# Optimization experiments

Measured on AMD Instinct MI355X. Metric: run time of the kernel, lower is better.

The kernel has to match this reference:

```python
import jax, jax.numpy as jnp
import numpy as np

H = 16  # n_heads


def setup_inputs() -> dict:
    key = jax.random.key(0)
    ks = jax.random.split(key, 11)
    B, S, D = 2, 2048, 1024
    def rn(k, shape, scale=1.0):
        return jax.random.normal(k, shape, dtype=jnp.float32) * scale
    w_scale = 1.0 / np.sqrt(D)
    return {
        "queries": rn(ks[0], (B, S, D)),
        "keys": rn(ks[1], (B, S, D)),
        "values": rn(ks[2], (B, S, D)),
        "Wq": rn(ks[3], (D, D), w_scale), "bq": rn(ks[4], (D,), 0.02),
        "Wk": rn(ks[5], (D, D), w_scale), "bk": rn(ks[6], (D,), 0.02),
        "Wv": rn(ks[7], (D, D), w_scale), "bv": rn(ks[8], (D,), 0.02),
        "Wo": rn(ks[9], (D, D), w_scale), "bo": rn(ks[10], (D,), 0.02),
    }


def _split_heads(x, h):
    # [B, S, D] -> [B, h, S, D/h]
    B, S, D = x.shape
    return x.reshape(B, S, h, D // h).transpose(0, 2, 1, 3)


def reference(queries, keys, values, Wq, bq, Wk, bk, Wv, bv, Wo, bo):
    B, S, D = queries.shape
    Q = _split_heads(queries @ Wq + bq, H)  # [B,h,S,dk]
    K = _split_heads(keys @ Wk + bk, H)
    V = _split_heads(values @ Wv + bv, H)
    # Faithful quirk: scale by sqrt(seq_len), not sqrt(d_k)
    factor = jnp.sqrt(jnp.asarray(S, dtype=Q.dtype))
    scores = jnp.einsum("bhqd,bhkd->bhqk", Q, K) / factor  # [B,h,S,S]
    weights = jax.nn.softmax(scores, axis=-1)
    attn = jnp.einsum("bhqk,bhkd->bhqd", weights, V)  # [B,h,S,dk]
    attn = attn.transpose(0, 2, 1, 3).reshape(B, S, D)  # [B,S,D]
    return attn @ Wo + bo
```

## Files before the change

### kernel.cpp

```cpp
#include <hip/hip_runtime.h>

typedef unsigned short ushort_t;
typedef unsigned int uint_t;
typedef __attribute__((ext_vector_type(8))) short short8;
typedef __attribute__((ext_vector_type(4))) float floatx4;

#define QSCALE 0.03187936f

__device__ __forceinline__ ushort_t f2bf(float f) {
    union { float f; uint_t u; } c; c.f = f;
    uint_t u = c.u;
    return (ushort_t)((u + 0x7fffu + ((u >> 16) & 1u)) >> 16);
}
__device__ __forceinline__ floatx4 mfma16x32(short8 a, short8 b, floatx4 c) {
    return __builtin_amdgcn_mfma_f32_16x16x32_bf16(a, b, c, 0, 0, 0);
}
__device__ __forceinline__ floatx4 zero4() { floatx4 z = {0.f, 0.f, 0.f, 0.f}; return z; }

__device__ __forceinline__ void gload16(const ushort_t* g, ushort_t* l) {
    __builtin_amdgcn_global_load_lds(
        (const __attribute__((address_space(1))) void*)g,
        (__attribute__((address_space(3))) void*)l, 16, 0, 0);
}

__global__ __launch_bounds__(256) void cvt_bf16(
    const float* __restrict__ s0, const float* __restrict__ s1,
    const float* __restrict__ s2, ushort_t* __restrict__ d0,
    ushort_t* __restrict__ d1, ushort_t* __restrict__ d2)
{
    const int which = blockIdx.x >> 11;
    const int blk = blockIdx.x & 2047;
    const float* src = (which == 0) ? s0 : (which == 1) ? s1 : s2;
    ushort_t* dst = (which == 0) ? d0 : (which == 1) ? d1 : d2;
    const int i = (blk * 256 + threadIdx.x) * 8;
    float4 f0 = *(const float4*)(src + i);
    float4 f1 = *(const float4*)(src + i + 4);
    __align__(16) ushort_t t[8];
    t[0] = f2bf(f0.x); t[1] = f2bf(f0.y); t[2] = f2bf(f0.z); t[3] = f2bf(f0.w);
    t[4] = f2bf(f1.x); t[5] = f2bf(f1.y); t[6] = f2bf(f1.z); t[7] = f2bf(f1.w);
    *(uint4*)(dst + i) = *(uint4*)t;
}

__global__ __launch_bounds__(256) void transpose_w(
    const float* __restrict__ W0, const float* __restrict__ W1,
    const float* __restrict__ W2, const float* __restrict__ W3,
    ushort_t* __restrict__ WT)
{
    __shared__ ushort_t tile[64][65];
    const float* W = (blockIdx.y == 0) ? W0 : (blockIdx.y == 1) ? W1
                   : (blockIdx.y == 2) ? W2 : W3;
    ushort_t* dst = WT + (size_t)blockIdx.y * (1024 * 1024);
    const int t = threadIdx.x;
    const int r = t >> 2, p = t & 3;
    const int j0 = (blockIdx.x & 15) << 6, k0 = (blockIdx.x >> 4) << 6;

    const float* src = W + (size_t)(k0 + r) * 1024 + j0 + p * 16;
    float4 f0 = *(const float4*)(src);
    float4 f1 = *(const float4*)(src + 4);
    float4 f2 = *(const float4*)(src + 8);
    float4 f3 = *(const float4*)(src + 12);
    ushort_t* tr = &tile[r][p * 16];
    tr[0] = f2bf(f0.x); tr[1] = f2bf(f0.y); tr[2]  = f2bf(f0.z); tr[3]  = f2bf(f0.w);
    tr[4] = f2bf(f1.x); tr[5] = f2bf(f1.y); tr[6]  = f2bf(f1.z); tr[7]  = f2bf(f1.w);
    tr[8] = f2bf(f2.x); tr[9] = f2bf(f2.y); tr[10] = f2bf(f2.z); tr[11] = f2bf(f2.w);
    tr[12] = f2bf(f3.x); tr[13] = f2bf(f3.y); tr[14] = f2bf(f3.z); tr[15] = f2bf(f3.w);
    __syncthreads();
    __align__(16) ushort_t buf[16];
#pragma unroll
    for (int i = 0; i < 16; ++i) buf[i] = tile[p * 16 + i][r];
    ushort_t* o = dst + (size_t)(j0 + r) * 1024 + k0 + p * 16;
    *(uint4*)(o)     = *(uint4*)(buf);
    *(uint4*)(o + 8) = *(uint4*)(buf + 8);
}

__global__ __launch_bounds__(256) void gemm_bt(
    const ushort_t* __restrict__ A0, const ushort_t* __restrict__ A1,
    const ushort_t* __restrict__ A2, const ushort_t* __restrict__ WT,
    const float* __restrict__ b0, const float* __restrict__ b1,
    const float* __restrict__ b2,
    ushort_t* __restrict__ Dq, ushort_t* __restrict__ Dk,
    ushort_t* __restrict__ Dv, int zbase)
{
    __shared__ __align__(16) ushort_t As[128 * 32];
    __shared__ __align__(16) ushort_t Bs[128 * 32];

    const int mode = blockIdx.z + zbase;
    const ushort_t* A = (mode == 0) ? A0 : (mode == 1) ? A1 : A2;
    const float* bias = (mode == 0) ? b0 : (mode == 1) ? b1 : b2;
    const ushort_t* Bt = WT + (size_t)mode * 1048576;

    const int tid = threadIdx.x;
    const int lane = tid & 63, wid = tid >> 6;
    const int quad = lane >> 4, l16 = lane & 15;
    const int wm = wid >> 1, wn = wid & 1;
    const int row0 = blockIdx.y << 7, col0 = blockIdx.x << 7;

    floatx4 acc[4][4];
#pragma unroll
    for (int i = 0; i < 4; ++i)
#pragma unroll
        for (int j = 0; j < 4; ++j) acc[i][j] = zero4();

    const int i0 = tid, i1 = 256 + tid;
    const int r0_ = i0 >> 2, c0_ = (i0 & 3) ^ (r0_ & 3);
    const int r1_ = i1 >> 2, c1_ = (i1 & 3) ^ (r1_ & 3);
    const ushort_t* gA0 = A  + (size_t)(row0 + r0_) * 1024 + c0_ * 8;
    const ushort_t* gA1 = A  + (size_t)(row0 + r1_) * 1024 + c1_ * 8;
    const ushort_t* gB0 = Bt + (size_t)(col0 + r0_) * 1024 + c0_ * 8;
    const ushort_t* gB1 = Bt + (size_t)(col0 + r1_) * 1024 + c1_ * 8;
    ushort_t* lA0 = As + i0 * 8;  ushort_t* lA1 = As + i1 * 8;
    ushort_t* lB0 = Bs + i0 * 8;  ushort_t* lB1 = Bs + i1 * 8;

    const int ra = wm * 64 + l16, rb = wn * 64 + l16;
    const int sa_off = (quad ^ (l16 & 3)) * 8;

    for (int k0 = 0; k0 < 1024; k0 += 32) {
        __syncthreads();
        gload16(gA0 + k0, lA0);
        gload16(gA1 + k0, lA1);
        gload16(gB0 + k0, lB0);
        gload16(gB1 + k0, lB1);
        __syncthreads();

        short8 af[4], bf[4];
#pragma unroll
        for (int i = 0; i < 4; ++i)
            af[i] = *(const short8*)(As + (ra + i * 16) * 32 + sa_off);
#pragma unroll
        for (int j = 0; j < 4; ++j)
            bf[j] = *(const short8*)(Bs + (rb + j * 16) * 32 + sa_off);
#pragma unroll
        for (int i = 0; i < 4; ++i)
#pragma unroll
            for (int j = 0; j < 4; ++j)
                acc[i][j] = mfma16x32(af[i], bf[j], acc[i][j]);
    }

    const float sc = (mode == 0) ? QSCALE : 1.f;
#pragma unroll
    for (int i = 0; i < 4; ++i) {
#pragma unroll
        for (int j = 0; j < 4; ++j) {
            const int c = col0 + wn * 64 + j * 16 + l16;
            const float bv = bias[c];
#pragma unroll
            for (int rr = 0; rr < 4; ++rr) {
                const int r = row0 + wm * 64 + i * 16 + quad * 4 + rr;
                const float v = (acc[i][j][rr] + bv) * sc;
                const int b = r >> 11, s = r & 2047, h = c >> 6, d = c & 63;
                if (mode <= 1) {
                    ushort_t* D = (mode == 0) ? Dq : Dk;
                    D[(((b * 16 + h) * 2048 + s) << 6) + d] = f2bf(v);
                } else {
                    Dv[(((b * 16 + h) * 64 + d) << 11) + s] = f2bf(v);
                }
            }
        }
    }
}

__global__ __launch_bounds__(256) void gemm64(
    const ushort_t* __restrict__ A, const ushort_t* __restrict__ Bt,
    const float* __restrict__ bias, float* __restrict__ Dout)
{
    __shared__ __align__(16) ushort_t As[64 * 32];
    __shared__ __align__(16) ushort_t Bs[128 * 32];
    const int tid = threadIdx.x;
    const int lane = tid & 63, wid = tid >> 6;
    const int quad = lane >> 4, l16 = lane & 15;
    const int wm = wid >> 1, wn = wid & 1;
    const int row0 = blockIdx.y << 6, col0 = blockIdx.x << 7;

    floatx4 acc[2][4];
#pragma unroll
    for (int i = 0; i < 2; ++i)
#pragma unroll
        for (int j = 0; j < 4; ++j) acc[i][j] = zero4();

    const int rA = tid >> 2, cA = (tid & 3) ^ (rA & 3);
    const ushort_t* gA = A + (size_t)(row0 + rA) * 1024 + cA * 8;
    ushort_t* lA = As + tid * 8;
    const int i0 = tid, i1 = 256 + tid;
    const int rB0 = i0 >> 2, cB0 = (i0 & 3) ^ (rB0 & 3);
    const int rB1 = i1 >> 2, cB1 = (i1 & 3) ^ (rB1 & 3);
    const ushort_t* gB0 = Bt + (size_t)(col0 + rB0) * 1024 + cB0 * 8;
    const ushort_t* gB1 = Bt + (size_t)(col0 + rB1) * 1024 + cB1 * 8;
    ushort_t* lB0 = Bs + i0 * 8;  ushort_t* lB1 = Bs + i1 * 8;

    const int sa_off = (quad ^ (l16 & 3)) * 8;

    for (int k0 = 0; k0 < 1024; k0 += 32) {
        __syncthreads();
        gload16(gA + k0, lA);
        gload16(gB0 + k0, lB0);
        gload16(gB1 + k0, lB1);
        __syncthreads();

        short8 af[2], bf[4];
#pragma unroll
        for (int i = 0; i < 2; ++i)
            af[i] = *(const short8*)(As + (wm * 32 + i * 16 + l16) * 32 + sa_off);
#pragma unroll
        for (int j = 0; j < 4; ++j)
            bf[j] = *(const short8*)(Bs + (wn * 64 + j * 16 + l16) * 32 + sa_off);
#pragma unroll
        for (int i = 0; i < 2; ++i)
#pragma unroll
            for (int j = 0; j < 4; ++j)
                acc[i][j] = mfma16x32(af[i], bf[j], acc[i][j]);
    }

#pragma unroll
    for (int i = 0; i < 2; ++i)
#pragma unroll
        for (int j = 0; j < 4; ++j) {
            const int c = col0 + wn * 64 + j * 16 + l16;
            const float bv = bias[c];
#pragma unroll
            for (int rr = 0; rr < 4; ++rr) {
                const int r = row0 + wm * 32 + i * 16 + quad * 4 + rr;
                Dout[(size_t)r * 1024 + c] = acc[i][j][rr] + bv;
            }
        }
}

__global__ __launch_bounds__(256, 4) void attn64(
    const ushort_t* __restrict__ Q, const ushort_t* __restrict__ K,
    const ushort_t* __restrict__ Vt, ushort_t* __restrict__ Out)
{
    __shared__ __align__(16) ushort_t Ks[64 * 64];
    __shared__ __align__(16) ushort_t Vs[64 * 64];

    const int tid = threadIdx.x;
    const int lane = tid & 63, wid = tid >> 6;
    const int quad = lane >> 4, l16 = lane & 15;
    const int bh = blockIdx.y;
    const int q0 = blockIdx.x << 6;

    const ushort_t* Qh = Q + (size_t)bh * (2048 * 64);
    const ushort_t* Kh = K + (size_t)bh * (2048 * 64);
    const ushort_t* Vh = Vt + (size_t)bh * (64 * 2048);

    const int qr = q0 + wid * 16 + l16;
    const short8 qf0 = *(const short8*)(Qh + (size_t)qr * 64 + quad * 8);
    const short8 qf1 = *(const short8*)(Qh + (size_t)qr * 64 + 32 + quad * 8);

    float l_st = 0.f;
    floatx4 o_acc[4];
#pragma unroll
    for (int d = 0; d < 4; ++d) o_acc[d] = zero4();

    const int i0 = tid, i1 = 256 + tid;
    const int kr0 = i0 >> 3, kc0 = (i0 & 7) ^ (kr0 & 7);
    const int kr1 = i1 >> 3, kc1 = (i1 & 7) ^ (kr1 & 7);
    const ushort_t* gK0 = Kh + (size_t)kr0 * 64 + kc0 * 8;
    const ushort_t* gK1 = Kh + (size_t)kr1 * 64 + kc1 * 8;
    const ushort_t* gV0 = Vh + (size_t)kr0 * 2048 + kc0 * 8;
    const ushort_t* gV1 = Vh + (size_t)kr1 * 2048 + kc1 * 8;
    ushort_t* lK0 = Ks + i0 * 8;  ushort_t* lK1 = Ks + i1 * 8;
    ushort_t* lV0 = Vs + i0 * 8;  ushort_t* lV1 = Vs + i1 * 8;

    const int l7 = l16 & 7;
    const int q2 = quad >> 1, q1 = (quad & 1) * 4;

    for (int kt = 0; kt < 2048; kt += 64) {
        __syncthreads();
        gload16(gK0 + (size_t)kt * 64, lK0);
        gload16(gK1 + (size_t)kt * 64, lK1);
        gload16(gV0 + kt, lV0);
        gload16(gV1 + kt, lV1);
        __syncthreads();

        floatx4 sa[4];
#pragma unroll
        for (int g = 0; g < 4; ++g) {
            const int row = g * 16 + l16;
            const short8 kf0 = *(const short8*)(Ks + row * 64 + ((quad ^ l7) * 8));
            const short8 kf1 = *(const short8*)(Ks + row * 64 + (((quad + 4) ^ l7) * 8));
            sa[g] = mfma16x32(kf0, qf0, zero4());
            sa[g] = mfma16x32(kf1, qf1, sa[g]);
        }

#pragma unroll
        for (int G = 0; G < 2; ++G) {
            uint_t ub[8];
#pragma unroll
            for (int t = 0; t < 8; ++t) {
                const int g = G * 2 + (t >> 2), r = t & 3;
                const float e = __builtin_amdgcn_exp2f(fminf(sa[g][r], 80.f));
                const uint_t u = __float_as_uint(e) & 0xffff0000u;
                l_st += __uint_as_float(u);
                ub[t] = u;
            }
            union { uint_t u[4]; short8 s; } pc;
            pc.u[0] = (ub[0] >> 16) | ub[1];
            pc.u[1] = (ub[2] >> 16) | ub[3];
            pc.u[2] = (ub[4] >> 16) | ub[5];
            pc.u[3] = (ub[6] >> 16) | ub[7];
            const short8 pf = pc.s;

            const int ch0 = ((4 * G + q2) ^ l7) * 8;
            const int ch1 = ((4 * G + 2 + q2) ^ l7) * 8;
#pragma unroll
            for (int db = 0; db < 4; ++db) {
                const int vbase = (db * 16 + l16) * 64 + q1;
                const uint2 v0 = *(const uint2*)(Vs + vbase + ch0);
                const uint2 v1 = *(const uint2*)(Vs + vbase + ch1);
                union { uint_t u[4]; short8 s; } vc;
                vc.u[0] = v0.x; vc.u[1] = v0.y; vc.u[2] = v1.x; vc.u[3] = v1.y;
                o_acc[db] = mfma16x32(pf, vc.s, o_acc[db]);
            }
        }
    }

    l_st += __shfl_xor(l_st, 16);
    l_st += __shfl_xor(l_st, 32);

    const int b = bh >> 4, h = bh & 15;
    const int s0 = q0 + wid * 16 + quad * 4;
#pragma unroll
    for (int r = 0; r < 4; ++r) {
        const float lr = __shfl(l_st, quad * 4 + r);
        const float inv = 1.f / lr;
#pragma unroll
        for (int db = 0; db < 4; ++db) {
            const float v = o_acc[db][r] * inv;
            Out[(size_t)(b * 2048 + s0 + r) * 1024 + h * 64 + db * 16 + l16] = f2bf(v);
        }
    }
}

extern "C" void kernel_launch(void* const* d_in, const int* in_sizes, int n_in,
                              void* d_out, int out_size, void* d_ws, size_t ws_size,
                              hipStream_t stream) {
    const float* queries = (const float*)d_in[0];
    const float* keys    = (const float*)d_in[1];
    const float* values  = (const float*)d_in[2];
    const float* Wq = (const float*)d_in[3];
    const float* bq = (const float*)d_in[4];
    const float* Wk = (const float*)d_in[5];
    const float* bk = (const float*)d_in[6];
    const float* Wv = (const float*)d_in[7];
    const float* bv = (const float*)d_in[8];
    const float* Wo = (const float*)d_in[9];
    const float* bo = (const float*)d_in[10];
    float* out = (float*)d_out;

    char* ws = (char*)d_ws;
    const size_t MB = 1024 * 1024;
    ushort_t* WT = (ushort_t*)(ws);
    const ushort_t* WoT = WT + 3 * 1048576;
    dim3 tb(256);

    transpose_w<<<dim3(256, 4), tb, 0, stream>>>(Wq, Wk, Wv, Wo, WT);

    if (ws_size >= 64 * MB) {
        ushort_t* Qb  = (ushort_t*)(ws + 8 * MB);
        ushort_t* Kb  = (ushort_t*)(ws + 16 * MB);
        ushort_t* Vb  = (ushort_t*)(ws + 24 * MB);
        ushort_t* Qp  = (ushort_t*)(ws + 32 * MB);
        ushort_t* Kp  = (ushort_t*)(ws + 40 * MB);
        ushort_t* Vtp = (ushort_t*)(ws + 48 * MB);
        ushort_t* An  = (ushort_t*)(ws + 56 * MB);
        cvt_bf16<<<dim3(6144), tb, 0, stream>>>(queries, keys, values, Qb, Kb, Vb);
        gemm_bt<<<dim3(8, 32, 3), tb, 0, stream>>>(Qb, Kb, Vb, WT,
            bq, bk, bv, Qp, Kp, Vtp, 0);
        attn64<<<dim3(32, 32), tb, 0, stream>>>(Qp, Kp, Vtp, An);
        gemm64<<<dim3(8, 64), tb, 0, stream>>>(An, WoT, bo, out);
    } else {
        ushort_t* buf1 = (ushort_t*)(ws + 8 * MB);
        ushort_t* buf2 = (ushort_t*)(ws + 16 * MB);
        ushort_t* Qp   = (ushort_t*)(ws + 24 * MB);
        ushort_t* Kp   = (ushort_t*)(ws + 32 * MB);
        cvt_bf16<<<dim3(4096), tb, 0, stream>>>(queries, keys, keys, buf1, buf2, buf2);
        gemm_bt<<<dim3(8, 32, 2), tb, 0, stream>>>(buf1, buf2, buf2, WT,
            bq, bk, bk, Qp, Kp, Kp, 0);
        cvt_bf16<<<dim3(2048), tb, 0, stream>>>(values, values, values, buf1, buf1, buf1);
        gemm_bt<<<dim3(8, 32, 1), tb, 0, stream>>>(buf1, buf1, buf1, WT,
            bv, bv, bv, buf2, buf2, buf2, 2);
        attn64<<<dim3(32, 32), tb, 0, stream>>>(Qp, Kp, buf2, buf1);
        gemm64<<<dim3(8, 64), tb, 0, stream>>>(buf1, WoT, bo, out);
    }
}
```

Before: 237.3 us.

## Unify projection GEMMs on 64x128 tiles and widen attention KV tile to 128

Result: slower. 305.5 us (+28.7%).

```diff
diff --git a/kernel.cpp b/kernel.cpp
--- a/kernel.cpp
+++ b/kernel.cpp
@@ -73,98 +73,23 @@
     *(uint4*)(o + 8) = *(uint4*)(buf + 8);
 }
 
-__global__ __launch_bounds__(256) void gemm_bt(
+__global__ __launch_bounds__(256) void gemm_nt64(
     const ushort_t* __restrict__ A0, const ushort_t* __restrict__ A1,
-    const ushort_t* __restrict__ A2, const ushort_t* __restrict__ WT,
+    const ushort_t* __restrict__ A2, const ushort_t* __restrict__ A3,
+    const ushort_t* __restrict__ WT,
     const float* __restrict__ b0, const float* __restrict__ b1,
-    const float* __restrict__ b2,
+    const float* __restrict__ b2, const float* __restrict__ b3,
     ushort_t* __restrict__ Dq, ushort_t* __restrict__ Dk,
-    ushort_t* __restrict__ Dv, int zbase)
-{
-    __shared__ __align__(16) ushort_t As[128 * 32];
-    __shared__ __align__(16) ushort_t Bs[128 * 32];
-
-    const int mode = blockIdx.z + zbase;
-    const ushort_t* A = (mode == 0) ? A0 : (mode == 1) ? A1 : A2;
-    const float* bias = (mode == 0) ? b0 : (mode == 1) ? b1 : b2;
-    const ushort_t* Bt = WT + (size_t)mode * 1048576;
-
-    const int tid = threadIdx.x;
-    const int lane = tid & 63, wid = tid >> 6;
-    const int quad = lane >> 4, l16 = lane & 15;
-    const int wm = wid >> 1, wn = wid & 1;
-    const int row0 = blockIdx.y << 7, col0 = blockIdx.x << 7;
-
-    floatx4 acc[4][4];
-#pragma unroll
-    for (int i = 0; i < 4; ++i)
-#pragma unroll
-        for (int j = 0; j < 4; ++j) acc[i][j] = zero4();
-
-    const int i0 = tid, i1 = 256 + tid;
-    const int r0_ = i0 >> 2, c0_ = (i0 & 3) ^ (r0_ & 3);
-    const int r1_ = i1 >> 2, c1_ = (i1 & 3) ^ (r1_ & 3);
-    const ushort_t* gA0 = A  + (size_t)(row0 + r0_) * 1024 + c0_ * 8;
-    const ushort_t* gA1 = A  + (size_t)(row0 + r1_) * 1024 + c1_ * 8;
-    const ushort_t* gB0 = Bt + (size_t)(col0 + r0_) * 1024 + c0_ * 8;
-    const ushort_t* gB1 = Bt + (size_t)(col0 + r1_) * 1024 + c1_ * 8;
-    ushort_t* lA0 = As + i0 * 8;  ushort_t* lA1 = As + i1 * 8;
-    ushort_t* lB0 = Bs + i0 * 8;  ushort_t* lB1 = Bs + i1 * 8;
-
-    const int ra = wm * 64 + l16, rb = wn * 64 + l16;
-    const int sa_off = (quad ^ (l16 & 3)) * 8;
-
-    for (int k0 = 0; k0 < 1024; k0 += 32) {
-        __syncthreads();
-        gload16(gA0 + k0, lA0);
-        gload16(gA1 + k0, lA1);
-        gload16(gB0 + k0, lB0);
-        gload16(gB1 + k0, lB1);
-        __syncthreads();
-
-        short8 af[4], bf[4];
-#pragma unroll
-        for (int i = 0; i < 4; ++i)
-            af[i] = *(const short8*)(As + (ra + i * 16) * 32 + sa_off);
-#pragma unroll
-        for (int j = 0; j < 4; ++j)
-            bf[j] = *(const short8*)(Bs + (rb + j * 16) * 32 + sa_off);
-#pragma unroll
-        for (int i = 0; i < 4; ++i)
-#pragma unroll
-            for (int j = 0; j < 4; ++j)
-                acc[i][j] = mfma16x32(af[i], bf[j], acc[i][j]);
-    }
-
-    const float sc = (mode == 0) ? QSCALE : 1.f;
-#pragma unroll
-    for (int i = 0; i < 4; ++i) {
-#pragma unroll
-        for (int j = 0; j < 4; ++j) {
-            const int c = col0 + wn * 64 + j * 16 + l16;
-            const float bv = bias[c];
-#pragma unroll
-            for (int rr = 0; rr < 4; ++rr) {
-                const int r = row0 + wm * 64 + i * 16 + quad * 4 + rr;
-                const float v = (acc[i][j][rr] + bv) * sc;
-                const int b = r >> 11, s = r & 2047, h = c >> 6, d = c & 63;
-                if (mode <= 1) {
-                    ushort_t* D = (mode == 0) ? Dq : Dk;
-                    D[(((b * 16 + h) * 2048 + s) << 6) + d] = f2bf(v);
-                } else {
-                    Dv[(((b * 16 + h) * 64 + d) << 11) + s] = f2bf(v);
-                }
-            }
-        }
-    }
-}
-
-__global__ __launch_bounds__(256) void gemm64(
-    const ushort_t* __restrict__ A, const ushort_t* __restrict__ Bt,
-    const float* __restrict__ bias, float* __restrict__ Dout)
+    ushort_t* __restrict__ Dv, float* __restrict__ Dout, int zbase)
 {
     __shared__ __align__(16) ushort_t As[64 * 32];
     __shared__ __align__(16) ushort_t Bs[128 * 32];
+
+    const int mode = blockIdx.z + zbase;
+    const ushort_t* A = (mode == 0) ? A0 : (mode == 1) ? A1 : (mode == 2) ? A2 : A3;
+    const float* bias = (mode == 0) ? b0 : (mode == 1) ? b1 : (mode == 2) ? b2 : b3;
+    const ushort_t* Bt = WT + (size_t)mode * 1048576;
+
     const int tid = threadIdx.x;
     const int lane = tid & 63, wid = tid >> 6;
     const int quad = lane >> 4, l16 = lane & 15;
@@ -210,8 +135,9 @@
                 acc[i][j] = mfma16x32(af[i], bf[j], acc[i][j]);
     }
 
-#pragma unroll
-    for (int i = 0; i < 2; ++i)
+    const float sc = (mode == 0) ? QSCALE : 1.f;
+#pragma unroll
+    for (int i = 0; i < 2; ++i) {
 #pragma unroll
         for (int j = 0; j < 4; ++j) {
             const int c = col0 + wn * 64 + j * 16 + l16;
@@ -219,23 +145,34 @@
 #pragma unroll
             for (int rr = 0; rr < 4; ++rr) {
                 const int r = row0 + wm * 32 + i * 16 + quad * 4 + rr;
-                Dout[(size_t)r * 1024 + c] = acc[i][j][rr] + bv;
+                const float v = (acc[i][j][rr] + bv) * sc;
+                const int b = r >> 11, s = r & 2047, h = c >> 6, d = c & 63;
+                if (mode <= 1) {
+                    ushort_t* D = (mode == 0) ? Dq : Dk;
+                    D[(((b * 16 + h) * 2048 + s) << 6) + d] = f2bf(v);
+                } else if (mode == 2) {
+                    Dv[(((b * 16 + h) * 64 + d) << 11) + s] = f2bf(v);
+                } else {
+                    Dout[(size_t)r * 1024 + c] = v;
+                }
             }
         }
+    }
 }
 
 __global__ __launch_bounds__(256, 4) void attn64(
     const ushort_t* __restrict__ Q, const ushort_t* __restrict__ K,
     const ushort_t* __restrict__ Vt, ushort_t* __restrict__ Out)
 {
-    __shared__ __align__(16) ushort_t Ks[64 * 64];
-    __shared__ __align__(16) ushort_t Vs[64 * 64];
+    __shared__ __align__(16) ushort_t Ks[128 * 64];
+    __shared__ __align__(16) ushort_t Vs[64 * 128];
 
     const int tid = threadIdx.x;
     const int lane = tid & 63, wid = tid >> 6;
     const int quad = lane >> 4, l16 = lane & 15;
-    const int bh = blockIdx.y;
-    const int q0 = blockIdx.x << 6;
+    const int blk = blockIdx.x;
+    const int bh = blk & 31;
+    const int q0 = (blk >> 5) << 6;
 
     const ushort_t* Qh = Q + (size_t)bh * (2048 * 64);
     const ushort_t* Kh = K + (size_t)bh * (2048 * 64);
@@ -250,30 +187,35 @@
 #pragma unroll
     for (int d = 0; d < 4; ++d) o_acc[d] = zero4();
 
-    const int i0 = tid, i1 = 256 + tid;
-    const int kr0 = i0 >> 3, kc0 = (i0 & 7) ^ (kr0 & 7);
-    const int kr1 = i1 >> 3, kc1 = (i1 & 7) ^ (kr1 & 7);
-    const ushort_t* gK0 = Kh + (size_t)kr0 * 64 + kc0 * 8;
-    const ushort_t* gK1 = Kh + (size_t)kr1 * 64 + kc1 * 8;
-    const ushort_t* gV0 = Vh + (size_t)kr0 * 2048 + kc0 * 8;
-    const ushort_t* gV1 = Vh + (size_t)kr1 * 2048 + kc1 * 8;
-    ushort_t* lK0 = Ks + i0 * 8;  ushort_t* lK1 = Ks + i1 * 8;
-    ushort_t* lV0 = Vs + i0 * 8;  ushort_t* lV1 = Vs + i1 * 8;
+    const ushort_t* gK[4]; const ushort_t* gV[4];
+    ushort_t *lK[4], *lV[4];
+#pragma unroll
+    for (int s = 0; s < 4; ++s) {
+        const int i = tid + 256 * s;
+        const int kr = i >> 3, kc = (i & 7) ^ (kr & 7);
+        gK[s] = Kh + (size_t)kr * 64 + kc * 8;
+        lK[s] = Ks + i * 8;
+        const int dr = i >> 4, cs = i & 15;
+        const int cc = (cs & 8) | ((cs & 7) ^ (dr & 7));
+        gV[s] = Vh + (size_t)dr * 2048 + cc * 8;
+        lV[s] = Vs + i * 8;
+    }
 
     const int l7 = l16 & 7;
     const int q2 = quad >> 1, q1 = (quad & 1) * 4;
 
-    for (int kt = 0; kt < 2048; kt += 64) {
+    for (int kt = 0; kt < 2048; kt += 128) {
         __syncthreads();
-        gload16(gK0 + (size_t)kt * 64, lK0);
-        gload16(gK1 + (size_t)kt * 64, lK1);
-        gload16(gV0 + kt, lV0);
-        gload16(gV1 + kt, lV1);
+#pragma unroll
+        for (int s = 0; s < 4; ++s) {
+            gload16(gK[s] + (size_t)kt * 64, lK[s]);
+            gload16(gV[s] + kt, lV[s]);
+        }
         __syncthreads();
 
-        floatx4 sa[4];
-#pragma unroll
-        for (int g = 0; g < 4; ++g) {
+        floatx4 sa[8];
+#pragma unroll
+        for (int g = 0; g < 8; ++g) {
             const int row = g * 16 + l16;
             const short8 kf0 = *(const short8*)(Ks + row * 64 + ((quad ^ l7) * 8));
             const short8 kf1 = *(const short8*)(Ks + row * 64 + (((quad + 4) ^ l7) * 8));
@@ -282,7 +224,7 @@
         }
 
 #pragma unroll
-        for (int G = 0; G < 2; ++G) {
+        for (int G = 0; G < 4; ++G) {
             uint_t ub[8];
 #pragma unroll
             for (int t = 0; t < 8; ++t) {
@@ -299,13 +241,14 @@
             pc.u[3] = (ub[6] >> 16) | ub[7];
             const short8 pf = pc.s;
 
-            const int ch0 = ((4 * G + q2) ^ l7) * 8;
-            const int ch1 = ((4 * G + 2 + q2) ^ l7) * 8;
+            const int c0 = 4 * G + q2, c1 = 4 * G + 2 + q2;
+            const int s0_ = ((c0 & 8) | ((c0 & 7) ^ l7)) * 8 + q1;
+            const int s1_ = ((c1 & 8) | ((c1 & 7) ^ l7)) * 8 + q1;
 #pragma unroll
             for (int db = 0; db < 4; ++db) {
-                const int vbase = (db * 16 + l16) * 64 + q1;
-                const uint2 v0 = *(const uint2*)(Vs + vbase + ch0);
-                const uint2 v1 = *(const uint2*)(Vs + vbase + ch1);
+                const int vbase = (db * 16 + l16) * 128;
+                const uint2 v0 = *(const uint2*)(Vs + vbase + s0_);
+                const uint2 v1 = *(const uint2*)(Vs + vbase + s1_);
                 union { uint_t u[4]; short8 s; } vc;
                 vc.u[0] = v0.x; vc.u[1] = v0.y; vc.u[2] = v1.x; vc.u[3] = v1.y;
                 o_acc[db] = mfma16x32(pf, vc.s, o_acc[db]);
@@ -349,7 +292,6 @@
     char* ws = (char*)d_ws;
     const size_t MB = 1024 * 1024;
     ushort_t* WT = (ushort_t*)(ws);
-    const ushort_t* WoT = WT + 3 * 1048576;
     dim3 tb(256);
 
     transpose_w<<<dim3(256, 4), tb, 0, stream>>>(Wq, Wk, Wv, Wo, WT);
@@ -363,22 +305,24 @@
         ushort_t* Vtp = (ushort_t*)(ws + 48 * MB);
         ushort_t* An  = (ushort_t*)(ws + 56 * MB);
         cvt_bf16<<<dim3(6144), tb, 0, stream>>>(queries, keys, values, Qb, Kb, Vb);
-        gemm_bt<<<dim3(8, 32, 3), tb, 0, stream>>>(Qb, Kb, Vb, WT,
-            bq, bk, bv, Qp, Kp, Vtp, 0);
-        attn64<<<dim3(32, 32), tb, 0, stream>>>(Qp, Kp, Vtp, An);
-        gemm64<<<dim3(8, 64), tb, 0, stream>>>(An, WoT, bo, out);
+        gemm_nt64<<<dim3(8, 64, 3), tb, 0, stream>>>(Qb, Kb, Vb, An, WT,
+            bq, bk, bv, bo, Qp, Kp, Vtp, out, 0);
+        attn64<<<dim3(1024), tb, 0, stream>>>(Qp, Kp, Vtp, An);
+        gemm_nt64<<<dim3(8, 64, 1), tb, 0, stream>>>(Qb, Kb, Vb, An, WT,
+            bq, bk, bv, bo, Qp, Kp, Vtp, out, 3);
     } else {
         ushort_t* buf1 = (ushort_t*)(ws + 8 * MB);
         ushort_t* buf2 = (ushort_t*)(ws + 16 * MB);
         ushort_t* Qp   = (ushort_t*)(ws + 24 * MB);
         ushort_t* Kp   = (ushort_t*)(ws + 32 * MB);
         cvt_bf16<<<dim3(4096), tb, 0, stream>>>(queries, keys, keys, buf1, buf2, buf2);
-        gemm_bt<<<dim3(8, 32, 2), tb, 0, stream>>>(buf1, buf2, buf2, WT,
-            bq, bk, bk, Qp, Kp, Kp, 0);
+        gemm_nt64<<<dim3(8, 64, 2), tb, 0, stream>>>(buf1, buf2, buf2, buf2, WT,
+            bq, bk, bk, bk, Qp, Kp, Kp, out, 0);
         cvt_bf16<<<dim3(2048), tb, 0, stream>>>(values, values, values, buf1, buf1, buf1);
-        gemm_bt<<<dim3(8, 32, 1), tb, 0, stream>>>(buf1, buf1, buf1, WT,
-            bv, bv, bv, buf2, buf2, buf2, 2);
-        attn64<<<dim3(32, 32), tb, 0, stream>>>(Qp, Kp, buf2, buf1);
-        gemm64<<<dim3(8, 64), tb, 0, stream>>>(buf1, WoT, bo, out);
-    }
-}
+        gemm_nt64<<<dim3(8, 64, 1), tb, 0, stream>>>(buf1, buf1, buf1, buf1, WT,
+            bv, bv, bv, bv, buf2, buf2, buf2, out, 2);
+        attn64<<<dim3(1024), tb, 0, stream>>>(Qp, Kp, buf2, buf1);
+        gemm_nt64<<<dim3(8, 64, 1), tb, 0, stream>>>(buf1, buf1, buf1, buf1, WT,
+            bo, bo, bo, bo, Qp, Kp, buf2, out, 3);
+    }
+}
```
